# Kernel tuning notes

Hardware: AMD Instinct MI355X
Metric: run time of the kernel (lower is better)

The kernel has to match this reference:

```python
import jax, jax.numpy as jnp
import numpy as np

B, CI, H, W = 128, 16, 32, 32
CO, K, S = 32, 3, 1
HO = (H - K) // S + 1  # 30
WO = (W - K) // S + 1  # 30
P = HO * WO  # 900 spatial locations
B_J0 = 0.1
DT = 0.5
BETA_ADAPT = 1.8  # is_adapt=True
BN_EPS = 1e-5


def setup_inputs() -> dict:
    key = jax.random.key(0)
    ks = jax.random.split(key, 16)
    inp = {
        'ff': jax.random.normal(ks[0], (B, CI, H, W), jnp.float32),
        'fb': jax.random.normal(ks[1], (B, CO, HO, WO), jnp.float32),
        'soma_t': jax.random.normal(ks[2], (B, CO, HO, WO), jnp.float32),
        'spk_t': (jax.random.uniform(ks[3], (B, CO, HO, WO)) > 0.7).astype(jnp.float32),
        'a_curr_t': jax.random.normal(ks[4], (B, CO, HO, WO), jnp.float32),
        'b_t': jax.random.uniform(ks[5], (B, CO, HO, WO), jnp.float32),
        # parameters
        'weight': jax.random.normal(ks[6], (1, CO, CI, HO, WO, K * K), jnp.float32) * 0.05,
        'conv_bias': jnp.zeros((1, CO, HO, WO), jnp.float32),
        'local_rec': jax.random.normal(ks[7], (P, CO, CO), jnp.float32) * (1.0 / np.sqrt(2.0 * CO)),
        'gamma': jnp.ones((CO,), jnp.float32),
        'beta': jnp.zeros((CO,), jnp.float32),
        'tau_m': 15.0 + 0.1 * jax.random.normal(ks[8], (CO, HO, WO), jnp.float32),
        'tau_adp': 20.0 + 0.1 * jax.random.normal(ks[9], (CO, HO, WO), jnp.float32),
        'tau_a': 15.0 + 0.1 * jax.random.normal(ks[10], (CO, HO, WO), jnp.float32),
    }
    return inp


def local_conv(x, weight, bias):
    # torch unfold(2,k).unfold(3,k) order: (kh, kw) fastest -> [B,Ci,Ho,Wo,k*k]
    patches = jnp.stack(
        [x[:, :, i:i + S * HO:S, j:j + S * WO:S] for i in range(K) for j in range(K)],
        axis=-1)
    out = jnp.einsum('bchwk,ochwk->bohw', patches, weight[0])
    return out + bias


def reference(ff, fb, soma_t, spk_t, a_curr_t, b_t, weight, conv_bias,
              local_rec, gamma, beta, tau_m, tau_adp, tau_a):
    # locally-connected conv + BatchNorm2d (training mode: batch stats)
    conv = local_conv(ff, weight, conv_bias)
    mean = conv.mean(axis=(0, 2, 3), keepdims=True)
    var = ((conv - mean) ** 2).mean(axis=(0, 2, 3), keepdims=True)  # biased var
    x = (conv - mean) * jax.lax.rsqrt(var + BN_EPS)
    conv_x = x * gamma[None, :, None, None] + beta[None, :, None, None]
    # recurrent per-location bmm: local_rec [P,Co,Co] @ spk [P,Co,B]
    spk_flat = spk_t.reshape(B, CO, P)
    rec = jnp.einsum('pij,bjp->bip', local_rec, spk_flat).reshape(B, CO, HO, WO)
    conv_x = conv_x + rec
    # adaptive LIF membrane update
    alpha = jnp.exp(-DT / tau_m)
    rho = jnp.exp(-DT / tau_adp)
    eta = jnp.exp(-DT / tau_a)
    b_new = rho * b_t + (1.0 - rho) * spk_t
    new_thre = B_J0 + BETA_ADAPT * b_new
    a_new = eta * a_curr_t + fb
    soma_new = alpha * soma_t + (jax.nn.sigmoid(a_new) - 0.5) + conv_x - new_thre * spk_t
    spike = (soma_new - new_thre > 0).astype(soma_new.dtype)
    return soma_new, spike, a_new, b_new
```

## Files before the change

kernel.cpp:

```cpp
#include <hip/hip_runtime.h>
#include <math.h>

#pragma clang fp contract(off)

#define B_   128
#define CI_  16
#define CO_  32
#define H_   32
#define W_   32
#define HO_  30
#define WO_  30
#define P_   900
#define CP_  (CO_*P_)
#define N_   ((size_t)B_*CP_)
#define NBLK_CONV (4*30*8)
#define WSTRIDE_O 129600
#define WSTRIDE_C 8100
#define FFC_ (H_*W_)
#define FFB_ (CI_*H_*W_)
#define FFTOT_ (B_*FFB_)


typedef __attribute__((address_space(1))) const unsigned int gas_uint;
typedef __attribute__((address_space(3))) unsigned int las_uint;
__device__ __forceinline__ void gload_lds4(const float* g, float* l) {
    __builtin_amdgcn_global_load_lds((gas_uint*)g, (las_uint*)l, 4, 0, 0);
}
__device__ __forceinline__ void gload_lds16(const float* g, float* l) {
    __builtin_amdgcn_global_load_lds((gas_uint*)g, (las_uint*)l, 16, 0, 0);
}

__global__ __launch_bounds__(256) void conv_kernel(
    const float* __restrict__ ff, const float* __restrict__ weight,
    const float* __restrict__ conv_bias, float* __restrict__ outf,
    double* __restrict__ part_sum, double* __restrict__ part_sumsq)
{
#pragma clang fp contract(off)
    const int tid = threadIdx.x;
    const int og  = (tid & 3) | ((tid >> 6) << 2);
    const int wg2 = (tid >> 2) & 3;
    const int bg  = (tid >> 4) & 3;
    const int wt = blockIdx.x;
    const int h  = blockIdx.y;
    const int b0 = blockIdx.z * 16;
    const int w0 = wt * 8 + wg2 * 2;
    const bool val = !(wt == 3 && wg2 == 3);
    const int wwave = tid & ~63;

    __shared__ float wg[2][2304];
    __shared__ float ffs[2][576];

    int wq_off[8];
#pragma unroll
    for (int q = 0; q < 8; ++q) {
        int s = q * 256 + tid;
        int ow = s >> 3, k = s & 7;
        int o = ow >> 3, w = ow & 7;
        int colc = wt * 8 + w; if (colc > 29) colc = 29;
        wq_off[q] = o * WSTRIDE_O + (h * WO_ + colc) * 9 + k;
    }
    int w8_off;
    {
        int o = tid >> 3, w = tid & 7;
        int colc = wt * 8 + w; if (colc > 29) colc = 29;
        w8_off = o * WSTRIDE_O + (h * WO_ + colc) * 9 + 8;
    }
    const bool fon = (tid < 144);
    int f_off = 0;
    if (fon) {
        int s0 = 4 * tid;
        int bb = s0 / 36, rm = s0 % 36, r = rm / 12, cc0 = rm % 12;
        f_off = (b0 + bb) * FFB_ + (h + r) * W_ + wt * 8 + cc0;
    }

    float acc[2][2][4];
#pragma unroll
    for (int oo = 0; oo < 2; ++oo)
#pragma unroll
        for (int ww = 0; ww < 2; ++ww)
#pragma unroll
            for (int j = 0; j < 4; ++j) acc[oo][ww][j] = 0.f;

    auto stage = [&](int c, int buf) {
        const float* wsrc = weight + c * WSTRIDE_C;
#pragma unroll
        for (int q = 0; q < 8; ++q)
            gload_lds4(wsrc + wq_off[q], &wg[buf][q * 256 + wwave]);
        gload_lds4(wsrc + w8_off, &wg[buf][2048 + wwave]);
        if (fon) {
            int g = f_off + c * FFC_;
            if (g > FFTOT_ - 4) g = FFTOT_ - 4;
            gload_lds16(ff + g, &ffs[buf][4 * wwave]);
        }
    };

    const int o0 = og * 2;
    auto compute_c = [&](int buf) {
        float wk[2][2][9];
#pragma unroll
        for (int oo = 0; oo < 2; ++oo)
#pragma unroll
            for (int ww = 0; ww < 2; ++ww) {
                const int ow = (o0 + oo) * 8 + wg2 * 2 + ww;
                const float4 a = *reinterpret_cast<const float4*>(&wg[buf][ow * 8]);
                const float4 b = *reinterpret_cast<const float4*>(&wg[buf][ow * 8 + 4]);
                wk[oo][ww][0] = a.x; wk[oo][ww][1] = a.y; wk[oo][ww][2] = a.z; wk[oo][ww][3] = a.w;
                wk[oo][ww][4] = b.x; wk[oo][ww][5] = b.y; wk[oo][ww][6] = b.z; wk[oo][ww][7] = b.w;
                wk[oo][ww][8] = wg[buf][2048 + ow];
            }
#pragma unroll
        for (int j = 0; j < 4; ++j) {
            const int bb = bg * 4 + j;
            float fr[3][4];
#pragma unroll
            for (int r = 0; r < 3; ++r) {
                const float2 u = *reinterpret_cast<const float2*>(&ffs[buf][bb * 36 + r * 12 + wg2 * 2]);
                const float2 v = *reinterpret_cast<const float2*>(&ffs[buf][bb * 36 + r * 12 + wg2 * 2 + 2]);
                fr[r][0] = u.x; fr[r][1] = u.y; fr[r][2] = v.x; fr[r][3] = v.y;
            }
#pragma unroll
            for (int oo = 0; oo < 2; ++oo)
#pragma unroll
                for (int ww = 0; ww < 2; ++ww) {
                    float a = acc[oo][ww][j];
#pragma unroll
                    for (int kh = 0; kh < 3; ++kh)
#pragma unroll
                        for (int kw = 0; kw < 3; ++kw) {
                            float prod = wk[oo][ww][kh * 3 + kw] * fr[kh][ww + kw];
                            a = a + prod;
                        }
                    acc[oo][ww][j] = a;
                }
        }
    };

    stage(0, 0);
    __syncthreads();
    for (int cs = 0; cs < CI_; cs += 2) {
        if (cs + 1 < CI_) stage(cs + 1, 1);
        compute_c(0);
        __syncthreads();
        if (cs + 2 < CI_) stage(cs + 2, 0);
        compute_c(1);
        __syncthreads();
    }

    double s1[2] = {0.0, 0.0}, s2[2] = {0.0, 0.0};
    if (val) {
#pragma unroll
        for (int oo = 0; oo < 2; ++oo) {
            const int o = o0 + oo;
            const int pidx = o * P_ + h * WO_ + w0;
            const float2 bi = *reinterpret_cast<const float2*>(conv_bias + pidx);
#pragma unroll
            for (int j = 0; j < 4; ++j) {
                const int b = b0 + bg * 4 + j;
                const size_t n = (size_t)b * CP_ + (size_t)pidx;
                float v0 = acc[oo][0][j] + bi.x;
                float v1 = acc[oo][1][j] + bi.y;
                *reinterpret_cast<float2*>(outf + 3 * N_ + n) = make_float2(v0, v1);
                double d0 = (double)v0, d1 = (double)v1;
                s1[oo] += d0; s2[oo] += d0 * d0;
                s1[oo] += d1; s2[oo] += d1 * d1;
            }
        }
    }
#pragma unroll
    for (int d = 4; d < 64; d <<= 1) {
#pragma unroll
        for (int oo = 0; oo < 2; ++oo) {
            s1[oo] += __shfl_xor(s1[oo], d);
            s2[oo] += __shfl_xor(s2[oo], d);
        }
    }
    if ((tid & 60) == 0) {
        int blk = (blockIdx.z * 30 + blockIdx.y) * 4 + blockIdx.x;
#pragma unroll
        for (int oo = 0; oo < 2; ++oo) {
            part_sum  [blk * CO_ + o0 + oo] = s1[oo];
            part_sumsq[blk * CO_ + o0 + oo] = s2[oo];
        }
    }
}

__global__ __launch_bounds__(256) void bn_finalize(
    const double* __restrict__ part_sum, const double* __restrict__ part_sumsq,
    float* __restrict__ Mb)
{
#pragma clang fp contract(off)
    const int o = blockIdx.x;
    const int tid = threadIdx.x;
    double s1 = 0.0, s2 = 0.0;
    for (int i = tid; i < NBLK_CONV; i += 256) {
        s1 += part_sum[i * CO_ + o];
        s2 += part_sumsq[i * CO_ + o];
    }
    __shared__ double r1[256], r2[256];
    r1[tid] = s1; r2[tid] = s2;
    __syncthreads();
    for (int s = 128; s > 0; s >>= 1) {
        if (tid < s) { r1[tid] += r1[tid + s]; r2[tid] += r2[tid + s]; }
        __syncthreads();
    }
    if (tid == 0) {
        const double cnt = (double)(B_ * (size_t)P_);
        double mean = r1[0] / cnt;
        float meanf = (float)mean;
        double md = (double)meanf;
        double var = r2[0] / cnt - 2.0 * md * (r1[0] / cnt) + md * md;
        float varf = (float)var;
        float invf = 1.0f / sqrtf(varf + 1e-5f);
        Mb[o]       = meanf;
        Mb[CO_ + o] = invf;
    }
}

__global__ __launch_bounds__(1024) void lif_rec_kernel(
    float* __restrict__ outf, const float* __restrict__ local_rec,
    const float* __restrict__ tau_m, const float* __restrict__ tau_adp,
    const float* __restrict__ tau_a, const float* __restrict__ Mb,
    const float* __restrict__ gamma, const float* __restrict__ beta,
    const float* __restrict__ fb, const float* __restrict__ soma_t,
    const float* __restrict__ spk_t, const float* __restrict__ a_curr,
    const float* __restrict__ b_t)
{
#pragma clang fp contract(off)
    const int tid = threadIdx.x;
    const int pp  = tid & 31;
    const int i   = tid >> 5;
    const int p   = blockIdx.x * 32 + pp;
    const bool pv = (p < P_);
    const int b0  = blockIdx.y * 8;

    float L[32];
    float meanf = 0.f, invf = 0.f, gm = 0.f, be = 0.f;
    float al = 0.f, rh = 0.f, et = 0.f;
    int rem = 0;
    if (pv) {
        const float4* lp = reinterpret_cast<const float4*>(local_rec + (size_t)p * (CO_ * CO_) + i * CO_);
#pragma unroll
        for (int q = 0; q < 8; ++q) {
            float4 v = lp[q];
            L[4 * q] = v.x; L[4 * q + 1] = v.y; L[4 * q + 2] = v.z; L[4 * q + 3] = v.w;
        }
        rem = i * P_ + p;
        meanf = Mb[i]; invf = Mb[CO_ + i];
        gm = gamma[i]; be = beta[i];
        al = expf(-0.5f / tau_m[rem]);
        rh = expf(-0.5f / tau_adp[rem]);
        et = expf(-0.5f / tau_a[rem]);
    }

    __shared__ float sp[2][CO_][32];

    size_t n = (size_t)b0 * CP_ + (size_t)rem;
    float sk_c = 0.f, cv_c = 0.f, bt_c = 0.f, ac_c = 0.f, fb_c = 0.f, so_c = 0.f;
    if (pv) {
        sk_c = spk_t[n]; cv_c = outf[3 * N_ + n]; bt_c = b_t[n];
        ac_c = a_curr[n]; fb_c = fb[n]; so_c = soma_t[n];
    }

#pragma unroll
    for (int bb = 0; bb < 8; ++bb) {
        const int cb = bb & 1;
        if (pv) sp[cb][i][pp] = sk_c;
        float sk_n = 0.f, cv_n = 0.f, bt_n = 0.f, ac_n = 0.f, fb_n = 0.f, so_n = 0.f;
        if (bb + 1 < 8 && pv) {
            const size_t nn = n + (size_t)CP_;
            sk_n = spk_t[nn]; cv_n = outf[3 * N_ + nn]; bt_n = b_t[nn];
            ac_n = a_curr[nn]; fb_n = fb[nn]; so_n = soma_t[nn];
        }
        asm volatile("s_waitcnt lgkmcnt(0)\n\ts_barrier" ::: "memory");
        if (pv) {
            float rec = 0.f;
#pragma unroll
            for (int j = 0; j < CO_; ++j) {
                float prod = L[j] * sp[cb][j][pp];
                rec = rec + prod;
            }

            float t  = cv_c - meanf;
            float x  = t * invf;
            float xg = x * gm;
            float cx = xg + be;
            cx = cx + rec;

            float rb  = rh * bt_c;
            float omr = 1.0f - rh;
            float os  = omr * sk_c;
            float bn  = rb + os;
            float tb = 1.8f * bn;
            float th = 0.1f + tb;
            float ea = et * ac_c;
            float an = ea + fb_c;
            float sg = 1.0f / (1.0f + expf(-an));
            float as = al * so_c;
            float s5 = sg - 0.5f;
            float u1 = as + s5;
            float u2 = u1 + cx;
            float ts = th * sk_c;
            float sn = u2 - ts;

            outf[n]          = sn;
            outf[N_ + n]     = ((sn - th) > 0.0f) ? 1.f : 0.f;
            outf[2 * N_ + n] = an;
            outf[3 * N_ + n] = bn;
        }
        sk_c = sk_n; cv_c = cv_n; bt_c = bt_n; ac_c = ac_n; fb_c = fb_n; so_c = so_n;
        n += (size_t)CP_;
    }
}

extern "C" void kernel_launch(void* const* d_in, const int* in_sizes, int n_in,
                              void* d_out, int out_size, void* d_ws, size_t ws_size,
                              hipStream_t stream)
{
    const float* ff        = (const float*)d_in[0];
    const float* fb        = (const float*)d_in[1];
    const float* soma_t    = (const float*)d_in[2];
    const float* spk_t     = (const float*)d_in[3];
    const float* a_curr    = (const float*)d_in[4];
    const float* b_t       = (const float*)d_in[5];
    const float* weight    = (const float*)d_in[6];
    const float* conv_bias = (const float*)d_in[7];
    const float* local_rec = (const float*)d_in[8];
    const float* gamma     = (const float*)d_in[9];
    const float* beta      = (const float*)d_in[10];
    const float* tau_m     = (const float*)d_in[11];
    const float* tau_adp   = (const float*)d_in[12];
    const float* tau_a     = (const float*)d_in[13];

    double* part_sum = (double*)d_ws;
    double* part_sq  = part_sum + (size_t)NBLK_CONV * CO_;
    float*  Mb       = (float*)(part_sq + (size_t)NBLK_CONV * CO_);

    float* outf = (float*)d_out;

    conv_kernel<<<dim3(4, 30, 8), 256, 0, stream>>>(
        ff, weight, conv_bias, outf, part_sum, part_sq);
    bn_finalize<<<dim3(CO_), 256, 0, stream>>>(part_sum, part_sq, Mb);
    lif_rec_kernel<<<dim3(29, 16), 1024, 0, stream>>>(
        outf, local_rec, tau_m, tau_adp, tau_a, Mb, gamma, beta,
        fb, soma_t, spk_t, a_curr, b_t);
}
```

Measured before the change: 123.6 us.

## Triple-buffer conv LDS staging with padded layout and partial vmcnt waits

Replaces the double-buffered weight/input staging with a three-stage ring buffer in one LDS array. Each iteration waits only for the older load group (vmcnt(9)) before a single barrier, so two channel loads stay in flight during compute. The weight tile layout is padded to a 68-float stride per output channel to cut LDS bank conflicts, and launch bounds request four blocks per CU. Risks include tighter register and LDS budgets and correctness depending on the hand-counted vmcnt matching the number of issued loads per stage.

New measurement: 348.8 us. +182.1%, slower.

```diff
diff --git a/kernel.cpp b/kernel.cpp
--- a/kernel.cpp
+++ b/kernel.cpp
@@ -20,6 +20,8 @@
 #define FFB_ (CI_*H_*W_)
 #define FFTOT_ (B_*FFB_)
 
+#define BUFSZ_ 3008
+
 
 typedef __attribute__((address_space(1))) const unsigned int gas_uint;
 typedef __attribute__((address_space(3))) unsigned int las_uint;
@@ -30,7 +32,7 @@
     __builtin_amdgcn_global_load_lds((gas_uint*)g, (las_uint*)l, 16, 0, 0);
 }
 
-__global__ __launch_bounds__(256) void conv_kernel(
+__global__ __launch_bounds__(256, 4) void conv_kernel(
     const float* __restrict__ ff, const float* __restrict__ weight,
     const float* __restrict__ conv_bias, float* __restrict__ outf,
     double* __restrict__ part_sum, double* __restrict__ part_sumsq)
@@ -40,22 +42,20 @@
     const int og  = (tid & 3) | ((tid >> 6) << 2);
     const int wg2 = (tid >> 2) & 3;
     const int bg  = (tid >> 4) & 3;
+    const int wave = tid >> 6;
     const int wt = blockIdx.x;
     const int h  = blockIdx.y;
     const int b0 = blockIdx.z * 16;
     const int w0 = wt * 8 + wg2 * 2;
     const bool val = !(wt == 3 && wg2 == 3);
-    const int wwave = tid & ~63;
-
-    __shared__ float wg[2][2304];
-    __shared__ float ffs[2][576];
+
+    __shared__ float lds[3 * BUFSZ_];
 
     int wq_off[8];
 #pragma unroll
     for (int q = 0; q < 8; ++q) {
         int s = q * 256 + tid;
-        int ow = s >> 3, k = s & 7;
-        int o = ow >> 3, w = ow & 7;
+        int o = s >> 6, w = (s >> 3) & 7, k = s & 7;
         int colc = wt * 8 + w; if (colc > 29) colc = 29;
         wq_off[q] = o * WSTRIDE_O + (h * WO_ + colc) * 9 + k;
     }
@@ -81,41 +81,43 @@
 #pragma unroll
             for (int j = 0; j < 4; ++j) acc[oo][ww][j] = 0.f;
 
-    auto stage = [&](int c, int buf) {
+    auto stage = [&](int c, float* buf) {
         const float* wsrc = weight + c * WSTRIDE_C;
 #pragma unroll
         for (int q = 0; q < 8; ++q)
-            gload_lds4(wsrc + wq_off[q], &wg[buf][q * 256 + wwave]);
-        gload_lds4(wsrc + w8_off, &wg[buf][2048 + wwave]);
+            gload_lds4(wsrc + wq_off[q], buf + (q * 4 + wave) * 68);
+        gload_lds4(wsrc + w8_off, buf + 2176 + (wave << 6));
         if (fon) {
             int g = f_off + c * FFC_;
             if (g > FFTOT_ - 4) g = FFTOT_ - 4;
-            gload_lds16(ff + g, &ffs[buf][4 * wwave]);
+            gload_lds16(ff + g, buf + 2432 + (wave << 8));
         }
     };
 
     const int o0 = og * 2;
-    auto compute_c = [&](int buf) {
+    auto compute_c = [&](const float* buf) {
         float wk[2][2][9];
 #pragma unroll
         for (int oo = 0; oo < 2; ++oo)
 #pragma unroll
             for (int ww = 0; ww < 2; ++ww) {
-                const int ow = (o0 + oo) * 8 + wg2 * 2 + ww;
-                const float4 a = *reinterpret_cast<const float4*>(&wg[buf][ow * 8]);
-                const float4 b = *reinterpret_cast<const float4*>(&wg[buf][ow * 8 + 4]);
+                const int o = o0 + oo, w = wg2 * 2 + ww;
+                const float* wp = buf + o * 68 + w * 8;
+                const float4 a = *reinterpret_cast<const float4*>(wp);
+                const float4 b = *reinterpret_cast<const float4*>(wp + 4);
                 wk[oo][ww][0] = a.x; wk[oo][ww][1] = a.y; wk[oo][ww][2] = a.z; wk[oo][ww][3] = a.w;
                 wk[oo][ww][4] = b.x; wk[oo][ww][5] = b.y; wk[oo][ww][6] = b.z; wk[oo][ww][7] = b.w;
-                wk[oo][ww][8] = wg[buf][2048 + ow];
+                wk[oo][ww][8] = buf[2176 + o * 8 + w];
             }
+        const float* fbase = buf + 2432;
 #pragma unroll
         for (int j = 0; j < 4; ++j) {
             const int bb = bg * 4 + j;
             float fr[3][4];
 #pragma unroll
             for (int r = 0; r < 3; ++r) {
-                const float2 u = *reinterpret_cast<const float2*>(&ffs[buf][bb * 36 + r * 12 + wg2 * 2]);
-                const float2 v = *reinterpret_cast<const float2*>(&ffs[buf][bb * 36 + r * 12 + wg2 * 2 + 2]);
+                const float2 u = *reinterpret_cast<const float2*>(fbase + bb * 36 + r * 12 + wg2 * 2);
+                const float2 v = *reinterpret_cast<const float2*>(fbase + bb * 36 + r * 12 + wg2 * 2 + 2);
                 fr[r][0] = u.x; fr[r][1] = u.y; fr[r][2] = v.x; fr[r][3] = v.y;
             }
 #pragma unroll
@@ -135,16 +137,20 @@
         }
     };
 
-    stage(0, 0);
-    __syncthreads();
-    for (int cs = 0; cs < CI_; cs += 2) {
-        if (cs + 1 < CI_) stage(cs + 1, 1);
-        compute_c(0);
-        __syncthreads();
-        if (cs + 2 < CI_) stage(cs + 2, 0);
-        compute_c(1);
-        __syncthreads();
-    }
+    float* pa = lds;
+    float* pb = lds + BUFSZ_;
+    float* pc = lds + 2 * BUFSZ_;
+    stage(0, pa);
+    stage(1, pb);
+#pragma unroll 3
+    for (int t = 0; t < CI_ - 1; ++t) {
+        asm volatile("s_waitcnt vmcnt(9)\n\ts_barrier" ::: "memory");
+        if (t + 2 < CI_) stage(t + 2, pc);
+        compute_c(pa);
+        float* tmp = pa; pa = pb; pb = pc; pc = tmp;
+    }
+    asm volatile("s_waitcnt vmcnt(0)\n\ts_barrier" ::: "memory");
+    compute_c(pa);
 
     double s1[2] = {0.0, 0.0}, s2[2] = {0.0, 0.0};
     if (val) {
```
